# Kernel optimization log

Hardware: AMD Instinct MI355X
Metric: run time of the kernel (lower is better)

## Reference

```python
import jax, jax.numpy as jnp
import numpy as np

B, S, D = 2, 2048, 1024
H = 16
KEY_DIM = 1024   # full projected dim; original scales by sqrt(key_dim), NOT head_dim
VAL_DIM = 1024
OUT_DIM = 1024


def setup_inputs() -> dict:
    key = jax.random.key(0)
    ks = jax.random.split(key, 11)
    s = 0.02
    return {
        "queries": jax.random.normal(ks[0], (B, S, D), jnp.float32),
        "keys": jax.random.normal(ks[1], (B, S, D), jnp.float32),
        "values": jax.random.normal(ks[2], (B, S, D), jnp.float32),
        "Wq": jax.random.normal(ks[3], (D, KEY_DIM), jnp.float32) * s,
        "bq": jnp.zeros((KEY_DIM,), jnp.float32),
        "Wk": jax.random.normal(ks[4], (D, KEY_DIM), jnp.float32) * s,
        "bk": jnp.zeros((KEY_DIM,), jnp.float32),
        "Wv": jax.random.normal(ks[5], (D, VAL_DIM), jnp.float32) * s,
        "bv": jnp.zeros((VAL_DIM,), jnp.float32),
        "Wo": jax.random.normal(ks[6], (KEY_DIM, OUT_DIM), jnp.float32) * s,
        "bo": jnp.zeros((OUT_DIM,), jnp.float32),
    }


def _split_heads(x):
    # [B, S, H*dh] -> [B, H, S, dh]
    b, s, _ = x.shape
    return x.reshape(b, s, H, -1).transpose(0, 2, 1, 3)


def reference(queries, keys, values, Wq, bq, Wk, bk, Wv, bv, Wo, bo):
    q = _split_heads(queries @ Wq + bq)   # [B,H,S,dk]
    k = _split_heads(keys @ Wk + bk)      # [B,H,S,dk]
    v = _split_heads(values @ Wv + bv)    # [B,H,S,dv]
    scale = jnp.sqrt(jnp.float32(KEY_DIM))  # full key_dim, as in the source
    scores = jnp.einsum('bhqd,bhkd->bhqk', q, k) / scale  # [B,H,S,S]
    # Source calls F.softmax with no dim; torch's legacy rule picks dim=1
    # (the heads axis) for a 4-D tensor. Reproduced faithfully.
    weights = jax.nn.softmax(scores, axis=1)
    o = jnp.einsum('bhqk,bhkd->bhqd', weights, v)          # [B,H,S,dv]
    o = o.transpose(0, 2, 1, 3).reshape(B, S, KEY_DIM)     # merge heads
    return o @ Wo + bo
```

## Files before the change

### kernel.cpp

```cpp
#include <hip/hip_runtime.h>


typedef unsigned short ushort;
typedef __attribute__((ext_vector_type(8))) short short8;
typedef __attribute__((ext_vector_type(4))) short short4v;
typedef __attribute__((ext_vector_type(4))) float f32x4;
typedef __attribute__((ext_vector_type(4))) float float4v;
typedef __attribute__((ext_vector_type(4))) unsigned int uint4v;
typedef __attribute__((ext_vector_type(2))) unsigned int uint2v;

#define MFMA32(a, b, c) __builtin_amdgcn_mfma_f32_16x16x32_bf16(a, b, c, 0, 0, 0)
#define MFMA16(a, b, c) __builtin_amdgcn_mfma_f32_16x16x16bf16_1k(a, b, c, 0, 0, 0)

__device__ __forceinline__ ushort f2bf(float f) {
    unsigned u = __float_as_uint(f);
    u += 0x7fffu + ((u >> 16) & 1u);
    return (ushort)(u >> 16);
}
__device__ __forceinline__ float bf2f(ushort u) {
    return __uint_as_float(((unsigned)u) << 16);
}

__device__ __forceinline__ void gload16(const ushort* g, ushort* l) {
    __builtin_amdgcn_global_load_lds(
        (__attribute__((address_space(1))) void*)(unsigned long long)(g),
        (__attribute__((address_space(3))) void*)(l), 16, 0, 0);
}

__global__ __launch_bounds__(256) void convert_x_kernel(
    const float* __restrict__ q, const float* __restrict__ k,
    const float* __restrict__ v, ushort* __restrict__ out) {
    const size_t NPER = 4194304ull;
    size_t idx = ((size_t)blockIdx.x * 256 + threadIdx.x) * 8;
    const size_t stride = (size_t)gridDim.x * 256 * 8;
    for (; idx < 3 * NPER; idx += stride) {
        const float* src;
        size_t off;
        if (idx < NPER)          { src = q; off = idx; }
        else if (idx < 2 * NPER) { src = k; off = idx - NPER; }
        else                     { src = v; off = idx - 2 * NPER; }
        float4v a = *(const float4v*)(src + off);
        float4v b = *(const float4v*)(src + off + 4);
        union { ushort u[8]; uint4v v4; } pk;
        #pragma unroll
        for (int j = 0; j < 4; j++) { pk.u[j] = f2bf(a[j]); pk.u[4 + j] = f2bf(b[j]); }
        *(uint4v*)(out + idx) = pk.v4;
    }
}

__global__ __launch_bounds__(256) void transpose_w_kernel(
    const float* __restrict__ w0, const float* __restrict__ w1,
    const float* __restrict__ w2, const float* __restrict__ w3,
    ushort* __restrict__ Wt) {
    const float* W = blockIdx.z == 0 ? w0 : blockIdx.z == 1 ? w1 : blockIdx.z == 2 ? w2 : w3;
    ushort* out = Wt + (size_t)blockIdx.z * 1024 * 1024;
    __shared__ ushort st[64 * 72];
    int t = threadIdx.x;
    int kb = blockIdx.y * 64, nb = blockIdx.x * 64;
    int c4 = (t & 15) * 4;
    int r0 = t >> 4;
    #pragma unroll
    for (int p = 0; p < 4; p++) {
        int r = r0 + p * 16;
        float4v f = *(const float4v*)(W + (size_t)(kb + r) * 1024 + nb + c4);
        union { ushort u[4]; uint2v v2; } pk;
        #pragma unroll
        for (int j = 0; j < 4; j++) pk.u[j] = f2bf(f[j]);
        *(uint2v*)(st + r * 72 + c4) = pk.v2;
    }
    __syncthreads();
    int n = t >> 2;
    int kc = (t & 3) * 16;
    union { ushort u[16]; uint4v v4[2]; } tw;
    #pragma unroll
    for (int j = 0; j < 16; j++) tw.u[j] = st[(kc + j) * 72 + n];
    uint4v* dst = (uint4v*)(out + (size_t)(nb + n) * 1024 + kb + kc);
    dst[0] = tw.v4[0];
    dst[1] = tw.v4[1];
}

__device__ __forceinline__ void gemm_core(
    const ushort* __restrict__ A, const ushort* __restrict__ Bt,
    const float* __restrict__ bias, ushort* __restrict__ Cb,
    float* __restrict__ Cf, int mode, ushort* sA, ushort* sB) {
    int tid = threadIdx.x, lane = tid & 63, wave = tid >> 6;
    int li = lane & 15, g = lane >> 4;
    int mt = blockIdx.y * 128, nt = blockIdx.x * 128;
    int wm = (wave >> 1) * 64, wn = (wave & 1) * 64;
    f32x4 acc[4][4] = {};
    for (int k0 = 0; k0 < 1024; k0 += 64) {
        __syncthreads();
        #pragma unroll
        for (int i = 0; i < 4; i++) {
            int c = tid + i * 256;
            int row = c >> 3, chd = c & 7;
            int cg = chd ^ (row & 7);
            gload16(A + (size_t)(mt + row) * 1024 + k0 + cg * 8, sA + c * 8);
            gload16(Bt + (size_t)(nt + row) * 1024 + k0 + cg * 8, sB + c * 8);
        }
        __syncthreads();
        #pragma unroll
        for (int kk = 0; kk < 2; kk++) {
            short8 af[4], bfr[4];
            #pragma unroll
            for (int i = 0; i < 4; i++) {
                int ra = wm + i * 16 + li;
                int cb = kk * 64 + g * 16;
                af[i] = *(const short8*)((char*)sA + ra * 128 + (cb ^ ((ra & 7) << 4)));
                int rb = wn + i * 16 + li;
                bfr[i] = *(const short8*)((char*)sB + rb * 128 + (cb ^ ((rb & 7) << 4)));
            }
            #pragma unroll
            for (int mi = 0; mi < 4; mi++)
                #pragma unroll
                for (int ni = 0; ni < 4; ni++)
                    acc[mi][ni] = MFMA32(af[mi], bfr[ni], acc[mi][ni]);
        }
    }
    #pragma unroll
    for (int mi = 0; mi < 4; mi++) {
        #pragma unroll
        for (int ni = 0; ni < 4; ni++) {
            int n = nt + wn + ni * 16 + li;
            int m0 = mt + wm + mi * 16 + g * 4;
            float bv = bias[n];
            if (mode == 0) {
                #pragma unroll
                for (int r = 0; r < 4; r++)
                    Cb[(size_t)(m0 + r) * 1024 + n] = f2bf(acc[mi][ni][r] + bv);
            } else if (mode == 1) {
                int batch = m0 >> 11, mm = m0 & 2047;
                union { ushort u[4]; uint2v v2; } pk;
                #pragma unroll
                for (int r = 0; r < 4; r++) pk.u[r] = f2bf(acc[mi][ni][r] + bv);
                *(uint2v*)(Cb + (size_t)batch * 1024 * 2048 + (size_t)n * 2048 + mm) = pk.v2;
            } else {
                #pragma unroll
                for (int r = 0; r < 4; r++)
                    Cf[(size_t)(m0 + r) * 1024 + n] = acc[mi][ni][r] + bv;
            }
        }
    }
}

__global__ __launch_bounds__(256, 2) void proj_kernel(
    const ushort* __restrict__ Xb, const ushort* __restrict__ Wt,
    const float* __restrict__ bq, const float* __restrict__ bk,
    const float* __restrict__ bv, ushort* __restrict__ Qb,
    ushort* __restrict__ Kb, ushort* __restrict__ Vtb) {
    __shared__ ushort sA[128 * 64];
    __shared__ ushort sB[128 * 64];
    int z = blockIdx.z;
    const float* bias = z == 0 ? bq : (z == 1 ? bk : bv);
    ushort* out = z == 0 ? Qb : (z == 1 ? Kb : Vtb);
    gemm_core(Xb + (size_t)z * 4194304ull, Wt + (size_t)z * 1048576ull,
              bias, out, nullptr, z == 2 ? 1 : 0, sA, sB);
}

__global__ __launch_bounds__(256, 2) void outproj_kernel(
    const ushort* __restrict__ Ob, const ushort* __restrict__ Wt3,
    const float* __restrict__ bo, float* __restrict__ out) {
    __shared__ ushort sA[128 * 64];
    __shared__ ushort sB[128 * 64];
    gemm_core(Ob, Wt3, bo, nullptr, out, 2, sA, sB);
}

__global__ __launch_bounds__(256, 4) void zsum_kernel(
    const ushort* __restrict__ Qb, const ushort* __restrict__ Kb,
    ushort* __restrict__ Zinv) {
    __shared__ ushort sQ[32 * 64];
    __shared__ ushort sK[128 * 64];
    int tid = threadIdx.x, lane = tid & 63, wave = tid >> 6;
    int li = lane & 15, g = lane >> 4;
    int b = blockIdx.z;
    int q0 = blockIdx.x * 32;
    int k0 = blockIdx.y * 128;
    const ushort* Qp = Qb + (size_t)(b * 2048 + q0) * 1024;
    const ushort* Kp = Kb + (size_t)(b * 2048 + k0) * 1024;
    int qr = tid >> 3, qc = tid & 7;
    int qcg = qc ^ (qr & 7);
    f32x4 zacc[2][2] = {};
    for (int h = 0; h < 16; h++) {
        int co = h * 64;
        __syncthreads();
        gload16(Qp + (size_t)qr * 1024 + co + qcg * 8, sQ + tid * 8);
        #pragma unroll
        for (int i = 0; i < 4; i++) {
            int c = tid + i * 256;
            int r = c >> 3, chd = c & 7;
            int cg = chd ^ (r & 7);
            gload16(Kp + (size_t)r * 1024 + co + cg * 8, sK + c * 8);
        }
        __syncthreads();
        short8 qf[2][2], kf[2][2];
        #pragma unroll
        for (int qs = 0; qs < 2; qs++)
            #pragma unroll
            for (int dc = 0; dc < 2; dc++) {
                int row = qs * 16 + li;
                qf[qs][dc] = *(const short8*)(
                    (char*)sQ + row * 128 + ((dc * 64 + g * 16) ^ ((row & 7) << 4)));
            }
        #pragma unroll
        for (int ks = 0; ks < 2; ks++)
            #pragma unroll
            for (int dc = 0; dc < 2; dc++) {
                int row = wave * 32 + ks * 16 + li;
                kf[ks][dc] = *(const short8*)(
                    (char*)sK + row * 128 + ((dc * 64 + g * 16) ^ ((row & 7) << 4)));
            }
        #pragma unroll
        for (int qs = 0; qs < 2; qs++)
            #pragma unroll
            for (int ks = 0; ks < 2; ks++) {
                f32x4 st = {0.f, 0.f, 0.f, 0.f};
                st = MFMA32(kf[ks][0], qf[qs][0], st);
                st = MFMA32(kf[ks][1], qf[qs][1], st);
                #pragma unroll
                for (int r = 0; r < 4; r++)
                    zacc[qs][ks][r] += __expf(st[r] * 0.03125f);
            }
    }
    #pragma unroll
    for (int qs = 0; qs < 2; qs++)
        #pragma unroll
        for (int ks = 0; ks < 2; ks++) {
            union { ushort u[4]; uint2v v; } pk;
            #pragma unroll
            for (int r = 0; r < 4; r++)
                pk.u[r] = f2bf(__builtin_amdgcn_rcpf(zacc[qs][ks][r]));
            *(uint2v*)(Zinv + (size_t)(b * 2048 + q0 + qs * 16 + li) * 2048 +
                       k0 + wave * 32 + ks * 16 + g * 4) = pk.v;
        }
}

__global__ __launch_bounds__(512, 2) void pv_kernel(
    const ushort* __restrict__ Qb, const ushort* __restrict__ Kb,
    const ushort* __restrict__ Vt, const ushort* __restrict__ Zinv,
    ushort* __restrict__ Ob) {
    __shared__ ushort sK[2 * 32 * 64];
    __shared__ ushort sV[2 * 64 * 32];
    __shared__ ushort sZ[64 * 32];
    int tid = threadIdx.x, lane = tid & 63, wave = tid >> 6;
    int li = lane & 15, g = lane >> 4;
    int b = blockIdx.y, hp = blockIdx.z;
    int q0 = blockIdx.x * 64;
    int hh = wave & 1, qg = wave >> 1;
    int head = hp * 2 + hh;
    short8 qf[2];
    #pragma unroll
    for (int dc = 0; dc < 2; dc++)
        qf[dc] = *(const short8*)(
            Qb + (size_t)(b * 2048 + q0 + qg * 16 + li) * 1024 +
            head * 64 + dc * 32 + g * 8);
    f32x4 oacc[4] = {};
    int kc_h2 = tid >> 8, kc_r = (tid >> 3) & 31, kc_c = tid & 7;
    int kc_cg = kc_c ^ (kc_r & 7);
    int vc_h2 = tid >> 8, vc_r = (tid >> 2) & 63, vc_c = tid & 3;
    int vc_cg = vc_c ^ (vc_r & 3);
    int zc_r = (tid & 255) >> 2, zc_c = tid & 3;
    int zc_cg = zc_c ^ (zc_r & 3);
    const ushort* Ksrc = Kb + (size_t)(b * 2048 + kc_r) * 1024 +
                         (hp * 2 + kc_h2) * 64 + kc_cg * 8;
    const ushort* Vsrc = Vt + (size_t)(b * 1024 + (hp * 2 + vc_h2) * 64 + vc_r) * 2048 +
                         vc_cg * 8;
    const ushort* Zsrc = Zinv + (size_t)(b * 2048 + q0 + zc_r) * 2048 + zc_cg * 8;
    ushort* Kdst = sK + tid * 8;
    ushort* Vdst = sV + tid * 8;
    ushort* Zdst = sZ + (tid & 255) * 8;
    int rw = qg * 16 + li;
    for (int kb = 0; kb < 2048; kb += 32) {
        __syncthreads();
        gload16(Ksrc + (size_t)kb * 1024, Kdst);
        gload16(Vsrc + kb, Vdst);
        if (tid < 256) gload16(Zsrc + kb, Zdst);
        __syncthreads();
        short8 kf[2][2];
        #pragma unroll
        for (int ks = 0; ks < 2; ks++)
            #pragma unroll
            for (int dc = 0; dc < 2; dc++) {
                int rk = ks * 16 + li;
                kf[ks][dc] = *(const short8*)(
                    (char*)sK + hh * 4096 + rk * 128 +
                    ((dc * 64 + g * 16) ^ ((rk & 7) << 4)));
            }
        f32x4 st[2];
        #pragma unroll
        for (int ks = 0; ks < 2; ks++) {
            f32x4 t0 = {0.f, 0.f, 0.f, 0.f};
            t0 = MFMA32(kf[ks][0], qf[0], t0);
            t0 = MFMA32(kf[ks][1], qf[1], t0);
            st[ks] = t0;
        }
        short4v pf[2];
        #pragma unroll
        for (int ks = 0; ks < 2; ks++) {
            int l = ks * 2 + (g >> 1);
            union { ushort u[4]; uint2v v; } rz;
            rz.v = *(const uint2v*)(
                (char*)sZ + rw * 64 + ((l ^ (rw & 3)) << 4) + (g & 1) * 8);
            short4v p;
            #pragma unroll
            for (int r = 0; r < 4; r++)
                p[r] = (short)f2bf(__expf(st[ks][r] * 0.03125f) * bf2f(rz.u[r]));
            pf[ks] = p;
        }
        #pragma unroll
        for (int ks = 0; ks < 2; ks++) {
            int l = ks * 2 + (g >> 1);
            #pragma unroll
            for (int ds = 0; ds < 4; ds++) {
                int rv = ds * 16 + li;
                short4v vf = *(const short4v*)(
                    (char*)sV + hh * 4096 + rv * 64 + ((l ^ (rv & 3)) << 4) + (g & 1) * 8);
                oacc[ds] = MFMA16(pf[ks], vf, oacc[ds]);
            }
        }
    }
    ushort* Oo = Ob + (size_t)(b * 2048 + q0 + qg * 16) * 1024 + head * 64;
    #pragma unroll
    for (int ds = 0; ds < 4; ds++)
        #pragma unroll
        for (int r = 0; r < 4; r++)
            Oo[(size_t)(g * 4 + r) * 1024 + ds * 16 + li] = f2bf(oacc[ds][r]);
}

extern "C" void kernel_launch(void* const* d_in, const int* in_sizes, int n_in,
                              void* d_out, int out_size, void* d_ws, size_t ws_size,
                              hipStream_t stream) {
    const float* queries = (const float*)d_in[0];
    const float* keys    = (const float*)d_in[1];
    const float* values  = (const float*)d_in[2];
    const float* Wq = (const float*)d_in[3];
    const float* bq = (const float*)d_in[4];
    const float* Wk = (const float*)d_in[5];
    const float* bk = (const float*)d_in[6];
    const float* Wv = (const float*)d_in[7];
    const float* bv = (const float*)d_in[8];
    const float* Wo = (const float*)d_in[9];
    const float* bo = (const float*)d_in[10];
    float* out = (float*)d_out;

    ushort* Xb  = (ushort*)d_ws;
    ushort* Wt  = Xb + 12ull * 1024 * 1024;
    ushort* Qb  = Wt + 4ull * 1024 * 1024;
    ushort* Kb  = Qb + 4ull * 1024 * 1024;
    ushort* Vtb = Kb + 4ull * 1024 * 1024;
    ushort* Zinv = Xb;
    ushort* Ob   = Xb + 8ull * 1024 * 1024;

    convert_x_kernel<<<2048, 256, 0, stream>>>(queries, keys, values, Xb);
    transpose_w_kernel<<<dim3(16, 16, 4), 256, 0, stream>>>(Wq, Wk, Wv, Wo, Wt);
    proj_kernel<<<dim3(8, 32, 3), 256, 0, stream>>>(Xb, Wt, bq, bk, bv, Qb, Kb, Vtb);
    zsum_kernel<<<dim3(64, 16, 2), 256, 0, stream>>>(Qb, Kb, Zinv);
    pv_kernel<<<dim3(32, 2, 8), 512, 0, stream>>>(Qb, Kb, Vtb, Zinv, Ob);
    outproj_kernel<<<dim3(8, 32), 256, 0, stream>>>(Ob, Wt + 3ull * 1024 * 1024, bo, out);
}
```

Before: 198.3 us.

## Retile zsum and pv kernels with larger tiles, double buffering, and block swizzle

zsum now handles 64 queries per block instead of 32, so each loaded K tile is reused across more query rows. pv_kernel is restructured so each wave owns one head with 32 queries (4 heads per block). It double-buffers the K, V and Z shared-memory tiles so the next stage's loads overlap the current compute, and uses one barrier per iteration. Both kernels use a 1D grid with block-index swizzling for locality. The cost is more registers and shared memory per block, which lowers occupancy, plus changed swizzle patterns in the Z and V layouts.

```diff
diff --git a/kernel.cpp b/kernel.cpp
--- a/kernel.cpp
+++ b/kernel.cpp
@@ -165,36 +165,40 @@
     gemm_core(Ob, Wt3, bo, nullptr, out, 2, sA, sB);
 }
 
-__global__ __launch_bounds__(256, 4) void zsum_kernel(
+__global__ __launch_bounds__(256, 2) void zsum_kernel(
     const ushort* __restrict__ Qb, const ushort* __restrict__ Kb,
     ushort* __restrict__ Zinv) {
-    __shared__ ushort sQ[32 * 64];
+    __shared__ ushort sQ[64 * 64];
     __shared__ ushort sK[128 * 64];
-    int tid = threadIdx.x, lane = tid & 63, wave = tid >> 6;
+    int tid = threadIdx.x, lane = tid & 63, wid = tid >> 6;
     int li = lane & 15, g = lane >> 4;
-    int b = blockIdx.z;
-    int q0 = blockIdx.x * 32;
-    int k0 = blockIdx.y * 128;
+    int bid = blockIdx.x;
+    int swz = (bid & 7) * 128 + (bid >> 3);
+    int qt = swz & 31, C = swz >> 5;
+    int b = C >> 4, kg = C & 15;
+    int q0 = qt * 64, k0 = kg * 128;
     const ushort* Qp = Qb + (size_t)(b * 2048 + q0) * 1024;
     const ushort* Kp = Kb + (size_t)(b * 2048 + k0) * 1024;
-    int qr = tid >> 3, qc = tid & 7;
-    int qcg = qc ^ (qr & 7);
-    f32x4 zacc[2][2] = {};
+    f32x4 zacc[4][2] = {};
     for (int h = 0; h < 16; h++) {
         int co = h * 64;
         __syncthreads();
-        gload16(Qp + (size_t)qr * 1024 + co + qcg * 8, sQ + tid * 8);
+        #pragma unroll
+        for (int i = 0; i < 2; i++) {
+            int c = tid + i * 256;
+            int r = c >> 3, m = c & 7;
+            gload16(Qp + (size_t)r * 1024 + co + (m ^ (r & 7)) * 8, sQ + c * 8);
+        }
         #pragma unroll
         for (int i = 0; i < 4; i++) {
             int c = tid + i * 256;
-            int r = c >> 3, chd = c & 7;
-            int cg = chd ^ (r & 7);
-            gload16(Kp + (size_t)r * 1024 + co + cg * 8, sK + c * 8);
-        }
-        __syncthreads();
-        short8 qf[2][2], kf[2][2];
-        #pragma unroll
-        for (int qs = 0; qs < 2; qs++)
+            int r = c >> 3, m = c & 7;
+            gload16(Kp + (size_t)r * 1024 + co + (m ^ (r & 7)) * 8, sK + c * 8);
+        }
+        __syncthreads();
+        short8 qf[4][2], kf[2][2];
+        #pragma unroll
+        for (int qs = 0; qs < 4; qs++)
             #pragma unroll
             for (int dc = 0; dc < 2; dc++) {
                 int row = qs * 16 + li;
@@ -205,12 +209,12 @@
         for (int ks = 0; ks < 2; ks++)
             #pragma unroll
             for (int dc = 0; dc < 2; dc++) {
-                int row = wave * 32 + ks * 16 + li;
+                int row = wid * 32 + ks * 16 + li;
                 kf[ks][dc] = *(const short8*)(
                     (char*)sK + row * 128 + ((dc * 64 + g * 16) ^ ((row & 7) << 4)));
             }
         #pragma unroll
-        for (int qs = 0; qs < 2; qs++)
+        for (int qs = 0; qs < 4; qs++)
             #pragma unroll
             for (int ks = 0; ks < 2; ks++) {
                 f32x4 st = {0.f, 0.f, 0.f, 0.f};
@@ -222,7 +226,7 @@
             }
     }
     #pragma unroll
-    for (int qs = 0; qs < 2; qs++)
+    for (int qs = 0; qs < 4; qs++)
         #pragma unroll
         for (int ks = 0; ks < 2; ks++) {
             union { ushort u[4]; uint2v v; } pk;
@@ -230,51 +234,59 @@
             for (int r = 0; r < 4; r++)
                 pk.u[r] = f2bf(__builtin_amdgcn_rcpf(zacc[qs][ks][r]));
             *(uint2v*)(Zinv + (size_t)(b * 2048 + q0 + qs * 16 + li) * 2048 +
-                       k0 + wave * 32 + ks * 16 + g * 4) = pk.v;
-        }
-}
-
-__global__ __launch_bounds__(512, 2) void pv_kernel(
+                       k0 + wid * 32 + ks * 16 + g * 4) = pk.v;
+        }
+}
+
+__global__ __launch_bounds__(256, 2) void pv_kernel(
     const ushort* __restrict__ Qb, const ushort* __restrict__ Kb,
     const ushort* __restrict__ Vt, const ushort* __restrict__ Zinv,
     ushort* __restrict__ Ob) {
-    __shared__ ushort sK[2 * 32 * 64];
-    __shared__ ushort sV[2 * 64 * 32];
-    __shared__ ushort sZ[64 * 32];
-    int tid = threadIdx.x, lane = tid & 63, wave = tid >> 6;
+    __shared__ ushort sK[2][4 * 32 * 64];
+    __shared__ ushort sV[2][4 * 64 * 32];
+    __shared__ ushort sZ[2][32 * 32];
+    int tid = threadIdx.x, lane = tid & 63, hh = tid >> 6;
     int li = lane & 15, g = lane >> 4;
-    int b = blockIdx.y, hp = blockIdx.z;
-    int q0 = blockIdx.x * 64;
-    int hh = wave & 1, qg = wave >> 1;
-    int head = hp * 2 + hh;
-    short8 qf[2];
-    #pragma unroll
-    for (int dc = 0; dc < 2; dc++)
-        qf[dc] = *(const short8*)(
-            Qb + (size_t)(b * 2048 + q0 + qg * 16 + li) * 1024 +
-            head * 64 + dc * 32 + g * 8);
-    f32x4 oacc[4] = {};
-    int kc_h2 = tid >> 8, kc_r = (tid >> 3) & 31, kc_c = tid & 7;
-    int kc_cg = kc_c ^ (kc_r & 7);
-    int vc_h2 = tid >> 8, vc_r = (tid >> 2) & 63, vc_c = tid & 3;
-    int vc_cg = vc_c ^ (vc_r & 3);
-    int zc_r = (tid & 255) >> 2, zc_c = tid & 3;
-    int zc_cg = zc_c ^ (zc_r & 3);
-    const ushort* Ksrc = Kb + (size_t)(b * 2048 + kc_r) * 1024 +
-                         (hp * 2 + kc_h2) * 64 + kc_cg * 8;
-    const ushort* Vsrc = Vt + (size_t)(b * 1024 + (hp * 2 + vc_h2) * 64 + vc_r) * 2048 +
-                         vc_cg * 8;
-    const ushort* Zsrc = Zinv + (size_t)(b * 2048 + q0 + zc_r) * 2048 + zc_cg * 8;
-    ushort* Kdst = sK + tid * 8;
-    ushort* Vdst = sV + tid * 8;
-    ushort* Zdst = sZ + (tid & 255) * 8;
-    int rw = qg * 16 + li;
-    for (int kb = 0; kb < 2048; kb += 32) {
-        __syncthreads();
-        gload16(Ksrc + (size_t)kb * 1024, Kdst);
-        gload16(Vsrc + kb, Vdst);
-        if (tid < 256) gload16(Zsrc + kb, Zdst);
-        __syncthreads();
+    int bid = blockIdx.x;
+    int swz = (bid & 7) * 64 + (bid >> 3);
+    int hp = swz & 3, p = swz >> 2;
+    int b = p >> 6, qt = p & 63;
+    int q0 = qt * 32;
+    int head = hp * 4 + hh;
+    short8 qf[2][2];
+    #pragma unroll
+    for (int qs = 0; qs < 2; qs++)
+        #pragma unroll
+        for (int dc = 0; dc < 2; dc++)
+            qf[qs][dc] = *(const short8*)(
+                Qb + (size_t)(b * 2048 + q0 + qs * 16 + li) * 1024 +
+                head * 64 + dc * 32 + g * 8);
+    f32x4 oacc[2][4] = {};
+    int kc_h = 0, kc_r = (tid >> 3) & 31, kc_m = tid & 7;
+    int vc_r = (tid >> 2) & 63, vc_m = tid & 3;
+    int zc_r = tid >> 2, zc_m = tid & 3;
+    const ushort* Kst = Kb + (size_t)(b * 2048 + kc_r) * 1024 + hp * 256 +
+                        (kc_m ^ (kc_r & 7)) * 8;
+    const ushort* Vst = Vt + (size_t)(b * 1024 + hp * 256 + vc_r) * 2048 +
+                        (vc_m ^ ((vc_r >> 1) & 3)) * 8;
+    const ushort* Zst = Zinv + (size_t)(b * 2048 + q0 + zc_r) * 2048 +
+                        (zc_m ^ ((zc_r >> 1) & 3)) * 8;
+    #define PV_STAGE(BUF, KB)                                                  \
+        {                                                                      \
+            _Pragma("unroll") for (int i = 0; i < 4; i++)                      \
+                gload16(Kst + (size_t)(KB) * 1024 + i * 64,                    \
+                        sK[BUF] + (tid + i * 256) * 8);                        \
+            _Pragma("unroll") for (int i = 0; i < 4; i++)                      \
+                gload16(Vst + (size_t)i * 64 * 2048 + (KB),                    \
+                        sV[BUF] + (tid + i * 256) * 8);                        \
+            if (tid < 128) gload16(Zst + (KB), sZ[BUF] + tid * 8);             \
+        }
+    PV_STAGE(0, 0)
+    __syncthreads();
+    for (int it = 0; it < 64; ++it) {
+        int cur = it & 1;
+        int kb = it * 32;
+        if (it + 1 < 64) PV_STAGE(cur ^ 1, kb + 32)
         short8 kf[2][2];
         #pragma unroll
         for (int ks = 0; ks < 2; ks++)
@@ -282,48 +294,54 @@
             for (int dc = 0; dc < 2; dc++) {
                 int rk = ks * 16 + li;
                 kf[ks][dc] = *(const short8*)(
-                    (char*)sK + hh * 4096 + rk * 128 +
+                    (char*)sK[cur] + hh * 4096 + rk * 128 +
                     ((dc * 64 + g * 16) ^ ((rk & 7) << 4)));
             }
-        f32x4 st[2];
+        short4v pf[2][2];
+        #pragma unroll
+        for (int qs = 0; qs < 2; qs++)
+            #pragma unroll
+            for (int ks = 0; ks < 2; ks++) {
+                f32x4 st = {0.f, 0.f, 0.f, 0.f};
+                st = MFMA32(kf[ks][0], qf[qs][0], st);
+                st = MFMA32(kf[ks][1], qf[qs][1], st);
+                int sl = ks * 4 + g;
+                int rq = qs * 16 + li;
+                union { ushort u[4]; uint2v v; } rz;
+                rz.v = *(const uint2v*)(
+                    (char*)sZ[cur] + rq * 64 +
+                    (((sl >> 1) ^ ((li >> 1) & 3)) * 2 + (sl & 1)) * 8);
+                short4v pp;
+                #pragma unroll
+                for (int r = 0; r < 4; r++)
+                    pp[r] = (short)f2bf(__expf(st[r] * 0.03125f) * bf2f(rz.u[r]));
+                pf[qs][ks] = pp;
+            }
         #pragma unroll
         for (int ks = 0; ks < 2; ks++) {
-            f32x4 t0 = {0.f, 0.f, 0.f, 0.f};
-            t0 = MFMA32(kf[ks][0], qf[0], t0);
-            t0 = MFMA32(kf[ks][1], qf[1], t0);
-            st[ks] = t0;
-        }
-        short4v pf[2];
-        #pragma unroll
-        for (int ks = 0; ks < 2; ks++) {
-            int l = ks * 2 + (g >> 1);
-            union { ushort u[4]; uint2v v; } rz;
-            rz.v = *(const uint2v*)(
-                (char*)sZ + rw * 64 + ((l ^ (rw & 3)) << 4) + (g & 1) * 8);
-            short4v p;
-            #pragma unroll
-            for (int r = 0; r < 4; r++)
-                p[r] = (short)f2bf(__expf(st[ks][r] * 0.03125f) * bf2f(rz.u[r]));
-            pf[ks] = p;
-        }
-        #pragma unroll
-        for (int ks = 0; ks < 2; ks++) {
-            int l = ks * 2 + (g >> 1);
+            int sl = ks * 4 + g;
             #pragma unroll
             for (int ds = 0; ds < 4; ds++) {
                 int rv = ds * 16 + li;
                 short4v vf = *(const short4v*)(
-                    (char*)sV + hh * 4096 + rv * 64 + ((l ^ (rv & 3)) << 4) + (g & 1) * 8);
-                oacc[ds] = MFMA16(pf[ks], vf, oacc[ds]);
-            }
-        }
-    }
-    ushort* Oo = Ob + (size_t)(b * 2048 + q0 + qg * 16) * 1024 + head * 64;
-    #pragma unroll
-    for (int ds = 0; ds < 4; ds++)
-        #pragma unroll
-        for (int r = 0; r < 4; r++)
-            Oo[(size_t)(g * 4 + r) * 1024 + ds * 16 + li] = f2bf(oacc[ds][r]);
+                    (char*)sV[cur] + hh * 4096 + rv * 64 +
+                    (((sl >> 1) ^ ((li >> 1) & 3)) * 2 + (sl & 1)) * 8);
+                oacc[0][ds] = MFMA16(pf[0][ks], vf, oacc[0][ds]);
+                oacc[1][ds] = MFMA16(pf[1][ks], vf, oacc[1][ds]);
+            }
+        }
+        __syncthreads();
+    }
+    #undef PV_STAGE
+    ushort* Oo = Ob + (size_t)(b * 2048 + q0) * 1024 + head * 64;
+    #pragma unroll
+    for (int qs = 0; qs < 2; qs++)
+        #pragma unroll
+        for (int ds = 0; ds < 4; ds++)
+            #pragma unroll
+            for (int r = 0; r < 4; r++)
+                Oo[(size_t)(qs * 16 + g * 4 + r) * 1024 + ds * 16 + li] =
+                    f2bf(oacc[qs][ds][r]);
 }
 
 extern "C" void kernel_launch(void* const* d_in, const int* in_sizes, int n_in,
@@ -353,7 +371,7 @@
     convert_x_kernel<<<2048, 256, 0, stream>>>(queries, keys, values, Xb);
     transpose_w_kernel<<<dim3(16, 16, 4), 256, 0, stream>>>(Wq, Wk, Wv, Wo, Wt);
     proj_kernel<<<dim3(8, 32, 3), 256, 0, stream>>>(Xb, Wt, bq, bk, bv, Qb, Kb, Vtb);
-    zsum_kernel<<<dim3(64, 16, 2), 256, 0, stream>>>(Qb, Kb, Zinv);
-    pv_kernel<<<dim3(32, 2, 8), 512, 0, stream>>>(Qb, Kb, Vtb, Zinv, Ob);
+    zsum_kernel<<<1024, 256, 0, stream>>>(Qb, Kb, Zinv);
+    pv_kernel<<<512, 256, 0, stream>>>(Qb, Kb, Vtb, Zinv, Ob);
     outproj_kernel<<<dim3(8, 32), 256, 0, stream>>>(Ob, Wt + 3ull * 1024 * 1024, bo, out);
 }
```

Result: no change. 194.9 us (-1.7%).
